# Kernel optimization log

Hardware: AMD Instinct MI355X
Metric: run time of the kernel (lower is better)

The kernel has to match this reference:

```python
import jax, jax.numpy as jnp
import numpy as np

NHEADS = 16

def setup_inputs() -> dict:
    key = jax.random.key(0)
    ks = jax.random.split(key, 11)
    B, S, D = 2, 2048, 1024
    std = 1.0 / np.sqrt(D)
    return {
        "query": jax.random.normal(ks[0], (B, S, D), jnp.float32),
        "key":   jax.random.normal(ks[1], (B, S, D), jnp.float32),
        "value": jax.random.normal(ks[2], (B, S, D), jnp.float32),
        "Wq": jax.random.normal(ks[3], (D, D), jnp.float32) * std,
        "bq": jax.random.normal(ks[4], (D,), jnp.float32) * std,
        "Wk": jax.random.normal(ks[5], (D, D), jnp.float32) * std,
        "bk": jax.random.normal(ks[6], (D,), jnp.float32) * std,
        "Wv": jax.random.normal(ks[7], (D, D), jnp.float32) * std,
        "bv": jax.random.normal(ks[8], (D,), jnp.float32) * std,
        "Wo": jax.random.normal(ks[9], (D, D), jnp.float32) * std,
        "bo": jax.random.normal(ks[10], (D,), jnp.float32) * std,
    }

def reference(query, key, value, Wq, bq, Wk, bk, Wv, bv, Wo, bo):
    B, Sq, D = query.shape
    Sk = key.shape[1]
    H = NHEADS
    hd = D // H
    q = (query @ Wq + bq).reshape(B, Sq, H, hd)
    k = (key @ Wk + bk).reshape(B, Sk, H, hd)
    v = (value @ Wv + bv).reshape(B, Sk, H, hd)
    # Explicit [B,H,Sq,Sk] score tensor, as in the original
    score = jnp.einsum('bqhd,bkhd->bhqk', q, k)
    # masked=True: causal mask applied before scaling (equivalent: -inf/c = -inf)
    cmask = jnp.triu(jnp.ones((Sq, Sk), dtype=bool), k=1)
    score = jnp.where(cmask, -jnp.inf, score)
    # NOTE: original divides by sqrt(score.shape[-1]) == sqrt(Sk), NOT sqrt(head_dim)
    scale = jnp.float32(1.0 / np.sqrt(Sk))
    att = jax.nn.softmax(score * scale, axis=-1)
    ret = jnp.einsum('bhqk,bkhd->bqhd', att, v).reshape(B, Sq, D)
    return ret @ Wo + bo
```

## Files before the change

kernel.cpp:

```cpp
#include <hip/hip_runtime.h>
#include <stdint.h>

typedef unsigned short u16;
typedef unsigned int u32;
typedef __bf16 bf16x8 __attribute__((ext_vector_type(8)));
typedef __bf16 bf16x4 __attribute__((ext_vector_type(4)));
typedef float f32x4 __attribute__((ext_vector_type(4)));

__device__ __forceinline__ u16 f2bf(float f) {
  u32 u = __float_as_uint(f);
  u = (u + 0x7fffu + ((u >> 16) & 1u)) >> 16;
  return (u16)u;
}

__device__ __forceinline__ void gload16(const void* g, void* l) {
  __builtin_amdgcn_global_load_lds(
      (const __attribute__((address_space(1))) void*)g,
      (__attribute__((address_space(3))) void*)l, 16, 0, 0);
}

__global__ __launch_bounds__(256) void prep_k(
    const float* __restrict__ q, const float* __restrict__ k,
    const float* __restrict__ v, u16* __restrict__ dst,
    const float* __restrict__ w0, const float* __restrict__ w1,
    const float* __restrict__ w2, const float* __restrict__ w3,
    u16* __restrict__ wt) {
  const int id = blockIdx.x;
  if (id < 6144) {
    const int y = id >> 11;
    const int x = id & 2047;
    const float* s = (y == 0) ? q : (y == 1) ? k : v;
    u16* d = dst + (size_t)y * 4194304u;
    int e = (x * 256 + threadIdx.x) * 8;
    float4 a = *(const float4*)(s + e);
    float4 b = *(const float4*)(s + e + 4);
    uint4 o;
    o.x = (u32)f2bf(a.x) | ((u32)f2bf(a.y) << 16);
    o.y = (u32)f2bf(a.z) | ((u32)f2bf(a.w) << 16);
    o.z = (u32)f2bf(b.x) | ((u32)f2bf(b.y) << 16);
    o.w = (u32)f2bf(b.z) | ((u32)f2bf(b.w) << 16);
    *(uint4*)(d + e) = o;
    return;
  }
  __shared__ float tile[64][65];
  const int t = id - 6144;
  const int z = t >> 8;
  const int rem = t & 255;
  const int x0 = (rem & 15) * 64, y0 = (rem >> 4) * 64;
  const float* W = (z == 0) ? w0 : (z == 1) ? w1 : (z == 2) ? w2 : w3;
  u16* Wt = wt + (size_t)z * 1048576u;
  const int tx = threadIdx.x & 63, ty = threadIdx.x >> 6;
#pragma unroll
  for (int j = 0; j < 16; ++j)
    tile[ty + j * 4][tx] = W[(size_t)(y0 + ty + j * 4) * 1024 + x0 + tx];
  __syncthreads();
#pragma unroll
  for (int j = 0; j < 16; ++j)
    Wt[(size_t)(x0 + ty + j * 4) * 1024 + y0 + tx] = f2bf(tile[tx][ty + j * 4]);
}

__global__ __launch_bounds__(256, 3) void gemm_proj(
    const u16* __restrict__ Xb, const u16* __restrict__ Wt,
    const float* __restrict__ bqp, const float* __restrict__ bkp,
    const float* __restrict__ bvp,
    u16* __restrict__ Qb, u16* __restrict__ Kb, u16* __restrict__ VtG,
    float qsc) {
  const int z = blockIdx.z;
  const u16 *A, *Bt;
  const float* bias;
  u16* C;
  int N, bm, bn;
  float osc = 1.f;
  bool rowb = false;
  if (z < 2) {
    A = Xb + (size_t)z * 4194304u;
    Bt = Wt + (size_t)z * 1048576u;
    bias = z ? bkp : bqp;
    C = z ? Kb : Qb;
    N = 1024;
    bm = blockIdx.x * 128;
    bn = blockIdx.y * 128;
    if (z == 0) osc = qsc;
  } else {
    A = Wt + 2u * 1048576u;
    Bt = Xb + 2u * 4194304u;
    bias = bvp;
    C = VtG;
    N = 4096;
    bm = blockIdx.y * 128;
    bn = blockIdx.x * 128;
    rowb = true;
  }

  __shared__ __align__(16) u16 ldsA[128 * 64];
  __shared__ __align__(16) u16 ldsB[128 * 64];

  const int tid = threadIdx.x;
  const int lane = tid & 63, wv = tid >> 6;
  const int wr = wv >> 1, wc = wv & 1;
  const int l15 = lane & 15, l4 = lane >> 4;

  const f32x4 zero4 = {0.f, 0.f, 0.f, 0.f};
  f32x4 acc[4][4];
#pragma unroll
  for (int i = 0; i < 4; ++i)
#pragma unroll
    for (int j = 0; j < 4; ++j) acc[i][j] = zero4;

  for (int kt = 0; kt < 16; ++kt) {
    __syncthreads();
#pragma unroll
    for (int g = 0; g < 4; ++g) {
      int p = g * 256 + tid;
      int row = p >> 3;
      int ss = (p & 7) ^ (row & 7);
      gload16(A + (size_t)(bm + row) * 1024 + kt * 64 + ss * 8,
              (char*)ldsA + (g * 256 + wv * 64) * 16);
    }
#pragma unroll
    for (int g = 0; g < 4; ++g) {
      int p = g * 256 + tid;
      int row = p >> 3;
      int ss = (p & 7) ^ (row & 7);
      gload16(Bt + (size_t)(bn + row) * 1024 + kt * 64 + ss * 8,
              (char*)ldsB + (g * 256 + wv * 64) * 16);
    }
    __syncthreads();

    bf16x8 af[4][2], bfr[4][2];
#pragma unroll
    for (int mf = 0; mf < 4; ++mf) {
      int row = wr * 64 + mf * 16 + l15;
#pragma unroll
      for (int ks = 0; ks < 2; ++ks) {
        int byt = row * 128 + ((ks * 64 + l4 * 16) ^ ((row & 7) << 4));
        af[mf][ks] = *(const bf16x8*)((const char*)ldsA + byt);
      }
    }
#pragma unroll
    for (int nf = 0; nf < 4; ++nf) {
      int row = wc * 64 + nf * 16 + l15;
#pragma unroll
      for (int ks = 0; ks < 2; ++ks) {
        int byt = row * 128 + ((ks * 64 + l4 * 16) ^ ((row & 7) << 4));
        bfr[nf][ks] = *(const bf16x8*)((const char*)ldsB + byt);
      }
    }
#pragma unroll
    for (int mf = 0; mf < 4; ++mf)
#pragma unroll
      for (int nf = 0; nf < 4; ++nf) {
        acc[mf][nf] = __builtin_amdgcn_mfma_f32_16x16x32_bf16(
            af[mf][0], bfr[nf][0], acc[mf][nf], 0, 0, 0);
        acc[mf][nf] = __builtin_amdgcn_mfma_f32_16x16x32_bf16(
            af[mf][1], bfr[nf][1], acc[mf][nf], 0, 0, 0);
      }
  }

  float bcol[4];
  if (!rowb) {
#pragma unroll
    for (int nf = 0; nf < 4; ++nf)
      bcol[nf] = bias[bn + wc * 64 + nf * 16 + l15];
  }
#pragma unroll
  for (int mf = 0; mf < 4; ++mf) {
#pragma unroll
    for (int i = 0; i < 4; ++i) {
      int r = bm + wr * 64 + mf * 16 + l4 * 4 + i;
      float br = rowb ? bias[r] : 0.f;
#pragma unroll
      for (int nf = 0; nf < 4; ++nf) {
        int c = bn + wc * 64 + nf * 16 + l15;
        float val = (acc[mf][nf][i] + (rowb ? br : bcol[nf])) * osc;
        C[(size_t)r * N + c] = f2bf(val);
      }
    }
  }
}

__global__ __launch_bounds__(256, 3) void gemm_out(
    const u16* __restrict__ A, const u16* __restrict__ Bt,
    const float* __restrict__ bias, float* __restrict__ C) {
  __shared__ __align__(16) u16 ldsA[128 * 64];
  __shared__ __align__(16) u16 ldsB[128 * 64];

  const int tid = threadIdx.x;
  const int lane = tid & 63, wv = tid >> 6;
  const int wr = wv >> 1, wc = wv & 1;
  const int l15 = lane & 15, l4 = lane >> 4;
  const int bm = blockIdx.x * 128, bn = blockIdx.y * 128;

  const f32x4 zero4 = {0.f, 0.f, 0.f, 0.f};
  f32x4 acc[4][4];
#pragma unroll
  for (int i = 0; i < 4; ++i)
#pragma unroll
    for (int j = 0; j < 4; ++j) acc[i][j] = zero4;

  for (int kt = 0; kt < 16; ++kt) {
    __syncthreads();
#pragma unroll
    for (int g = 0; g < 4; ++g) {
      int p = g * 256 + tid;
      int row = p >> 3;
      int ss = (p & 7) ^ (row & 7);
      gload16(A + (size_t)(bm + row) * 1024 + kt * 64 + ss * 8,
              (char*)ldsA + (g * 256 + wv * 64) * 16);
    }
#pragma unroll
    for (int g = 0; g < 4; ++g) {
      int p = g * 256 + tid;
      int row = p >> 3;
      int ss = (p & 7) ^ (row & 7);
      gload16(Bt + (size_t)(bn + row) * 1024 + kt * 64 + ss * 8,
              (char*)ldsB + (g * 256 + wv * 64) * 16);
    }
    __syncthreads();

    bf16x8 af[4][2], bfr[4][2];
#pragma unroll
    for (int mf = 0; mf < 4; ++mf) {
      int row = wr * 64 + mf * 16 + l15;
#pragma unroll
      for (int ks = 0; ks < 2; ++ks) {
        int byt = row * 128 + ((ks * 64 + l4 * 16) ^ ((row & 7) << 4));
        af[mf][ks] = *(const bf16x8*)((const char*)ldsA + byt);
      }
    }
#pragma unroll
    for (int nf = 0; nf < 4; ++nf) {
      int row = wc * 64 + nf * 16 + l15;
#pragma unroll
      for (int ks = 0; ks < 2; ++ks) {
        int byt = row * 128 + ((ks * 64 + l4 * 16) ^ ((row & 7) << 4));
        bfr[nf][ks] = *(const bf16x8*)((const char*)ldsB + byt);
      }
    }
#pragma unroll
    for (int mf = 0; mf < 4; ++mf)
#pragma unroll
      for (int nf = 0; nf < 4; ++nf) {
        acc[mf][nf] = __builtin_amdgcn_mfma_f32_16x16x32_bf16(
            af[mf][0], bfr[nf][0], acc[mf][nf], 0, 0, 0);
        acc[mf][nf] = __builtin_amdgcn_mfma_f32_16x16x32_bf16(
            af[mf][1], bfr[nf][1], acc[mf][nf], 0, 0, 0);
      }
  }

  float bcol[4];
#pragma unroll
  for (int nf = 0; nf < 4; ++nf)
    bcol[nf] = bias[bn + wc * 64 + nf * 16 + l15];
#pragma unroll
  for (int mf = 0; mf < 4; ++mf) {
#pragma unroll
    for (int i = 0; i < 4; ++i) {
      int r = bm + wr * 64 + mf * 16 + l4 * 4 + i;
#pragma unroll
      for (int nf = 0; nf < 4; ++nf) {
        int c = bn + wc * 64 + nf * 16 + l15;
        C[(size_t)r * 1024 + c] = acc[mf][nf][i] + bcol[nf];
      }
    }
  }
}

__global__ __launch_bounds__(256, 4) void attn_k(
    const u16* __restrict__ Q, const u16* __restrict__ Kb,
    const u16* __restrict__ Vt, u16* __restrict__ ctx) {
  const int id = blockIdx.x + (blockIdx.y << 5);
  const int xcd = id & 7;
  const int kk = id >> 3;
  const int bh = xcd * 4 + (kk & 3);
  const int qt = 31 - (kk >> 2);
  const int b = bh >> 4, h = bh & 15;
  const int tid = threadIdx.x;
  const int lane = tid & 63, wv = tid >> 6;
  const int l15 = lane & 15, l4 = lane >> 4;

  __shared__ __align__(16) u16 Kt[2][64 * 64];
  __shared__ __align__(16) u16 Vl[2][64 * 64];
  __shared__ __align__(16) u16 Pl[4][16 * 64];

  const u16* KB = Kb + (size_t)(b * 2048) * 1024 + h * 64;
  const u16* VB = Vt + (size_t)(h * 64) * 4096 + b * 2048;

  const u16* qp =
      Q + (size_t)(b * 2048 + qt * 64 + wv * 16 + l15) * 1024 + h * 64;
  bf16x8 qf0 = *(const bf16x8*)(qp + l4 * 8);
  bf16x8 qf1 = *(const bf16x8*)(qp + 32 + l4 * 8);

  const f32x4 zero4 = {0.f, 0.f, 0.f, 0.f};
  f32x4 oacc[4];
#pragma unroll
  for (int i = 0; i < 4; ++i) oacc[i] = zero4;
  float m = -1e30f, lsum = 0.f;

  auto issueKV = [&](int jt, int bufi) {
    const u16* kb = KB + (size_t)(jt * 64) * 1024;
#pragma unroll
    for (int g = 0; g < 2; ++g) {
      int p = g * 256 + tid;
      int row = p >> 3;
      int ss = (p & 7) ^ (row & 7);
      gload16(kb + (size_t)row * 1024 + ss * 8,
              (char*)(&Kt[bufi][0]) + (g * 256 + wv * 64) * 16);
    }
#pragma unroll
    for (int g = 0; g < 2; ++g) {
      int p = g * 256 + tid;
      int d = p >> 3;
      int ss = (p & 7) ^ (d & 7);
      gload16(VB + (size_t)d * 4096 + jt * 64 + ss * 8,
              (char*)(&Vl[bufi][0]) + (g * 256 + wv * 64) * 16);
    }
  };

  issueKV(0, 0);
  for (int j = 0; j <= qt; ++j) {
    const int cur = j & 1;
    __syncthreads();
    if (j < qt) issueKV(j + 1, cur ^ 1);

    f32x4 p4[4];
    __builtin_amdgcn_s_setprio(1);
#pragma unroll
    for (int nt = 0; nt < 4; ++nt) {
      int row = nt * 16 + l15;
      int sw = (row & 7) << 4;
      const char* kr = (const char*)&Kt[cur][0] + row * 128;
      bf16x8 k0 = *(const bf16x8*)(kr + ((l4 * 16) ^ sw));
      bf16x8 k1 = *(const bf16x8*)(kr + ((64 + l4 * 16) ^ sw));
      f32x4 s = zero4;
      s = __builtin_amdgcn_mfma_f32_16x16x32_bf16(k0, qf0, s, 0, 0, 0);
      s = __builtin_amdgcn_mfma_f32_16x16x32_bf16(k1, qf1, s, 0, 0, 0);
      p4[nt] = s;
    }
    __builtin_amdgcn_s_setprio(0);

    if (j == qt) {
#pragma unroll
      for (int nt = 0; nt < 4; ++nt)
#pragma unroll
        for (int i = 0; i < 4; ++i)
          if (nt * 16 + l4 * 4 + i > wv * 16 + l15) p4[nt][i] = -1e30f;
    }

    float rm = p4[0][0];
#pragma unroll
    for (int nt = 0; nt < 4; ++nt)
#pragma unroll
      for (int i = 0; i < 4; ++i) rm = fmaxf(rm, p4[nt][i]);
    rm = fmaxf(rm, __shfl_xor(rm, 16, 64));
    rm = fmaxf(rm, __shfl_xor(rm, 32, 64));

    if (!__all(rm - m <= 8.0f)) {
      float mn = fmaxf(m, rm);
      float ce = exp2f(m - mn);
      m = mn;
      lsum *= ce;
#pragma unroll
      for (int i = 0; i < 4; ++i) {
        float cei = __shfl(ce, (lane & 48) | (l4 * 4 + i), 64);
#pragma unroll
        for (int nt = 0; nt < 4; ++nt) oacc[nt][i] *= cei;
      }
    }

    float rs = 0.f;
#pragma unroll
    for (int nt = 0; nt < 4; ++nt)
#pragma unroll
      for (int i = 0; i < 4; ++i) {
        float e = exp2f(p4[nt][i] - m);
        p4[nt][i] = e;
        rs += e;
      }
    rs += __shfl_xor(rs, 16, 64);
    rs += __shfl_xor(rs, 32, 64);
    lsum += rs;

    {
      int sw = (l15 & 7) << 4;
#pragma unroll
      for (int nt = 0; nt < 4; ++nt) {
        bf16x4 pb = __builtin_convertvector(p4[nt], bf16x4);
        *(bf16x4*)((char*)&Pl[wv][0] + l15 * 128 + ((nt * 32 + l4 * 8) ^ sw)) = pb;
      }
    }

    bf16x8 pa0, pa1;
    {
      int sw = (l15 & 7) << 4;
      pa0 = *(const bf16x8*)((const char*)&Pl[wv][0] + l15 * 128 + ((l4 * 16) ^ sw));
      pa1 = *(const bf16x8*)((const char*)&Pl[wv][0] + l15 * 128 +
                             ((64 + l4 * 16) ^ sw));
    }
    __builtin_amdgcn_s_setprio(1);
#pragma unroll
    for (int nt = 0; nt < 4; ++nt) {
      int d = nt * 16 + l15;
      int sw = (d & 7) << 4;
      const char* vr = (const char*)&Vl[cur][0] + d * 128;
      bf16x8 v0 = *(const bf16x8*)(vr + ((l4 * 16) ^ sw));
      bf16x8 v1 = *(const bf16x8*)(vr + ((64 + l4 * 16) ^ sw));
      oacc[nt] = __builtin_amdgcn_mfma_f32_16x16x32_bf16(pa0, v0, oacc[nt], 0, 0, 0);
      oacc[nt] = __builtin_amdgcn_mfma_f32_16x16x32_bf16(pa1, v1, oacc[nt], 0, 0, 0);
    }
    __builtin_amdgcn_s_setprio(0);
  }

  float rcp = 1.f / lsum;
  u16* cb = ctx + (size_t)(b * 2048 + qt * 64 + wv * 16) * 1024 + h * 64;
#pragma unroll
  for (int i = 0; i < 4; ++i) {
    float iv = __shfl(rcp, (lane & 48) | (l4 * 4 + i), 64);
    int r = l4 * 4 + i;
#pragma unroll
    for (int nt = 0; nt < 4; ++nt)
      cb[(size_t)r * 1024 + nt * 16 + l15] = f2bf(oacc[nt][i] * iv);
  }
}

extern "C" void kernel_launch(void* const* d_in, const int* in_sizes, int n_in,
                              void* d_out, int out_size, void* d_ws,
                              size_t ws_size, hipStream_t stream) {
  const float* q  = (const float*)d_in[0];
  const float* k  = (const float*)d_in[1];
  const float* v  = (const float*)d_in[2];
  const float* Wq = (const float*)d_in[3];
  const float* bq = (const float*)d_in[4];
  const float* Wk = (const float*)d_in[5];
  const float* bk = (const float*)d_in[6];
  const float* Wv = (const float*)d_in[7];
  const float* bv = (const float*)d_in[8];
  const float* Wo = (const float*)d_in[9];
  const float* bo = (const float*)d_in[10];

  char* ws = (char*)d_ws;
  u16* Xb  = (u16*)ws;
  u16* Wt  = (u16*)(ws + 25165824);
  u16* VtG = (u16*)(ws + 33554432);
  u16* ctx = Xb;
  u16* Qb  = (u16*)d_out;
  u16* Kb  = Qb + 4194304;

  const float SC2A = 0.0318793585f;

  prep_k<<<dim3(7168), 256, 0, stream>>>(q, k, v, Xb, Wq, Wk, Wv, Wo, Wt);
  gemm_proj<<<dim3(32, 8, 3), 256, 0, stream>>>(Xb, Wt, bq, bk, bv, Qb, Kb,
                                                VtG, SC2A);
  attn_k<<<dim3(32, 32), 256, 0, stream>>>(Qb, Kb, VtG, ctx);
  gemm_out<<<dim3(32, 8), 256, 0, stream>>>(ctx, Wt + 3 * 1048576, bo,
                                            (float*)d_out);
}
```

Before: 114.2 us.

## Load K and V fragments directly from global memory instead of LDS staging

Removes the double-buffered LDS staging of K and V tiles (async global-to-LDS copies plus a barrier per iteration) and has each wave read its MFMA operand fragments straight from global memory. This drops the per-iteration __syncthreads and the LDS footprint, which could raise occupancy. In exchange, the four waves of a block each fetch the same K/V data separately, relying on cache, and the loads are no longer prefetched ahead of the compute, which exposes global-memory latency.

```diff
diff --git a/kernel.cpp b/kernel.cpp
--- a/kernel.cpp
+++ b/kernel.cpp
@@ -279,8 +279,6 @@
   const int lane = tid & 63, wv = tid >> 6;
   const int l15 = lane & 15, l4 = lane >> 4;
 
-  __shared__ __align__(16) u16 Kt[2][64 * 64];
-  __shared__ __align__(16) u16 Vl[2][64 * 64];
   __shared__ __align__(16) u16 Pl[4][16 * 64];
 
   const u16* KB = Kb + (size_t)(b * 2048) * 1024 + h * 64;
@@ -297,41 +295,14 @@
   for (int i = 0; i < 4; ++i) oacc[i] = zero4;
   float m = -1e30f, lsum = 0.f;
 
-  auto issueKV = [&](int jt, int bufi) {
-    const u16* kb = KB + (size_t)(jt * 64) * 1024;
-#pragma unroll
-    for (int g = 0; g < 2; ++g) {
-      int p = g * 256 + tid;
-      int row = p >> 3;
-      int ss = (p & 7) ^ (row & 7);
-      gload16(kb + (size_t)row * 1024 + ss * 8,
-              (char*)(&Kt[bufi][0]) + (g * 256 + wv * 64) * 16);
-    }
-#pragma unroll
-    for (int g = 0; g < 2; ++g) {
-      int p = g * 256 + tid;
-      int d = p >> 3;
-      int ss = (p & 7) ^ (d & 7);
-      gload16(VB + (size_t)d * 4096 + jt * 64 + ss * 8,
-              (char*)(&Vl[bufi][0]) + (g * 256 + wv * 64) * 16);
-    }
-  };
-
-  issueKV(0, 0);
   for (int j = 0; j <= qt; ++j) {
-    const int cur = j & 1;
-    __syncthreads();
-    if (j < qt) issueKV(j + 1, cur ^ 1);
-
     f32x4 p4[4];
     __builtin_amdgcn_s_setprio(1);
 #pragma unroll
     for (int nt = 0; nt < 4; ++nt) {
-      int row = nt * 16 + l15;
-      int sw = (row & 7) << 4;
-      const char* kr = (const char*)&Kt[cur][0] + row * 128;
-      bf16x8 k0 = *(const bf16x8*)(kr + ((l4 * 16) ^ sw));
-      bf16x8 k1 = *(const bf16x8*)(kr + ((64 + l4 * 16) ^ sw));
+      const u16* kr = KB + (size_t)(j * 64 + nt * 16 + l15) * 1024;
+      bf16x8 k0 = *(const bf16x8*)(kr + l4 * 8);
+      bf16x8 k1 = *(const bf16x8*)(kr + 32 + l4 * 8);
       f32x4 s = zero4;
       s = __builtin_amdgcn_mfma_f32_16x16x32_bf16(k0, qf0, s, 0, 0, 0);
       s = __builtin_amdgcn_mfma_f32_16x16x32_bf16(k1, qf1, s, 0, 0, 0);
@@ -400,11 +371,9 @@
     __builtin_amdgcn_s_setprio(1);
 #pragma unroll
     for (int nt = 0; nt < 4; ++nt) {
-      int d = nt * 16 + l15;
-      int sw = (d & 7) << 4;
-      const char* vr = (const char*)&Vl[cur][0] + d * 128;
-      bf16x8 v0 = *(const bf16x8*)(vr + ((l4 * 16) ^ sw));
-      bf16x8 v1 = *(const bf16x8*)(vr + ((64 + l4 * 16) ^ sw));
+      const u16* vr = VB + (size_t)(nt * 16 + l15) * 4096 + j * 64;
+      bf16x8 v0 = *(const bf16x8*)(vr + l4 * 8);
+      bf16x8 v1 = *(const bf16x8*)(vr + 32 + l4 * 8);
       oacc[nt] = __builtin_amdgcn_mfma_f32_16x16x32_bf16(pa0, v0, oacc[nt], 0, 0, 0);
       oacc[nt] = __builtin_amdgcn_mfma_f32_16x16x32_bf16(pa1, v1, oacc[nt], 0, 0, 0);
     }
```

Measured after the change: 210.7 us. 84.5% more time.

## Pair causal query tiles per block to balance work and share K/V loads

Applied to the files above, without the earlier changes.

Each attention block now handles two query tiles, qtA and its mirror 31-qtA, so every block does the same total causal work. The K/V tiles it loads are reused by both tiles for the shared prefix. The grid is halved to 512 blocks and launch bounds drop to 2 blocks per CU to make room for the doubled accumulators. This removes the tail imbalance of causal tiles and cuts redundant K/V traffic, at the cost of fewer resident waves and higher register pressure.

```diff
diff --git a/kernel.cpp b/kernel.cpp
--- a/kernel.cpp
+++ b/kernel.cpp
@@ -266,14 +266,15 @@
   }
 }
 
-__global__ __launch_bounds__(256, 4) void attn_k(
+__global__ __launch_bounds__(256, 2) void attn_k(
     const u16* __restrict__ Q, const u16* __restrict__ Kb,
     const u16* __restrict__ Vt, u16* __restrict__ ctx) {
-  const int id = blockIdx.x + (blockIdx.y << 5);
+  const int id = blockIdx.x + (blockIdx.y << 4);
   const int xcd = id & 7;
   const int kk = id >> 3;
   const int bh = xcd * 4 + (kk & 3);
-  const int qt = 31 - (kk >> 2);
+  const int qtA = kk >> 2;
+  const int qtB = 31 - qtA;
   const int b = bh >> 4, h = bh & 15;
   const int tid = threadIdx.x;
   const int lane = tid & 63, wv = tid >> 6;
@@ -286,16 +287,20 @@
   const u16* KB = Kb + (size_t)(b * 2048) * 1024 + h * 64;
   const u16* VB = Vt + (size_t)(h * 64) * 4096 + b * 2048;
 
-  const u16* qp =
-      Q + (size_t)(b * 2048 + qt * 64 + wv * 16 + l15) * 1024 + h * 64;
-  bf16x8 qf0 = *(const bf16x8*)(qp + l4 * 8);
-  bf16x8 qf1 = *(const bf16x8*)(qp + 32 + l4 * 8);
+  const u16* qpa =
+      Q + (size_t)(b * 2048 + qtA * 64 + wv * 16 + l15) * 1024 + h * 64;
+  const u16* qpb =
+      Q + (size_t)(b * 2048 + qtB * 64 + wv * 16 + l15) * 1024 + h * 64;
+  bf16x8 qa0 = *(const bf16x8*)(qpa + l4 * 8);
+  bf16x8 qa1 = *(const bf16x8*)(qpa + 32 + l4 * 8);
+  bf16x8 qb0 = *(const bf16x8*)(qpb + l4 * 8);
+  bf16x8 qb1 = *(const bf16x8*)(qpb + 32 + l4 * 8);
 
   const f32x4 zero4 = {0.f, 0.f, 0.f, 0.f};
-  f32x4 oacc[4];
-#pragma unroll
-  for (int i = 0; i < 4; ++i) oacc[i] = zero4;
-  float m = -1e30f, lsum = 0.f;
+  f32x4 oA[4], oB[4];
+#pragma unroll
+  for (int i = 0; i < 4; ++i) { oA[i] = zero4; oB[i] = zero4; }
+  float mA = -1e30f, lsA = 0.f, mB = -1e30f, lsB = 0.f;
 
   auto issueKV = [&](int jt, int bufi) {
     const u16* kb = KB + (size_t)(jt * 64) * 1024;
@@ -317,12 +322,8 @@
     }
   };
 
-  issueKV(0, 0);
-  for (int j = 0; j <= qt; ++j) {
-    const int cur = j & 1;
-    __syncthreads();
-    if (j < qt) issueKV(j + 1, cur ^ 1);
-
+  auto computeTile = [&](int cur, bool diag, bf16x8 qf0, bf16x8 qf1,
+                         float& m, float& lsum, f32x4* oacc) {
     f32x4 p4[4];
     __builtin_amdgcn_s_setprio(1);
 #pragma unroll
@@ -339,7 +340,7 @@
     }
     __builtin_amdgcn_s_setprio(0);
 
-    if (j == qt) {
+    if (diag) {
 #pragma unroll
       for (int nt = 0; nt < 4; ++nt)
 #pragma unroll
@@ -409,17 +410,32 @@
       oacc[nt] = __builtin_amdgcn_mfma_f32_16x16x32_bf16(pa1, v1, oacc[nt], 0, 0, 0);
     }
     __builtin_amdgcn_s_setprio(0);
-  }
-
-  float rcp = 1.f / lsum;
-  u16* cb = ctx + (size_t)(b * 2048 + qt * 64 + wv * 16) * 1024 + h * 64;
+  };
+
+  issueKV(0, 0);
+  for (int j = 0; j <= qtB; ++j) {
+    const int cur = j & 1;
+    __syncthreads();
+    if (j < qtB) issueKV(j + 1, cur ^ 1);
+    computeTile(cur, j == qtB, qb0, qb1, mB, lsB, oB);
+    if (j <= qtA) computeTile(cur, j == qtA, qa0, qa1, mA, lsA, oA);
+  }
+
+  float rcpA = 1.f / lsA;
+  float rcpB = 1.f / lsB;
+  u16* ca = ctx + (size_t)(b * 2048 + qtA * 64 + wv * 16) * 1024 + h * 64;
+  u16* cb = ctx + (size_t)(b * 2048 + qtB * 64 + wv * 16) * 1024 + h * 64;
 #pragma unroll
   for (int i = 0; i < 4; ++i) {
-    float iv = __shfl(rcp, (lane & 48) | (l4 * 4 + i), 64);
+    int src = (lane & 48) | (l4 * 4 + i);
+    float ivA = __shfl(rcpA, src, 64);
+    float ivB = __shfl(rcpB, src, 64);
     int r = l4 * 4 + i;
 #pragma unroll
-    for (int nt = 0; nt < 4; ++nt)
-      cb[(size_t)r * 1024 + nt * 16 + l15] = f2bf(oacc[nt][i] * iv);
+    for (int nt = 0; nt < 4; ++nt) {
+      ca[(size_t)r * 1024 + nt * 16 + l15] = f2bf(oA[nt][i] * ivA);
+      cb[(size_t)r * 1024 + nt * 16 + l15] = f2bf(oB[nt][i] * ivB);
+    }
   }
 }
 
@@ -451,7 +467,7 @@
   prep_k<<<dim3(7168), 256, 0, stream>>>(q, k, v, Xb, Wq, Wk, Wv, Wo, Wt);
   gemm_proj<<<dim3(32, 8, 3), 256, 0, stream>>>(Xb, Wt, bq, bk, bv, Qb, Kb,
                                                 VtG, SC2A);
-  attn_k<<<dim3(32, 32), 256, 0, stream>>>(Qb, Kb, VtG, ctx);
+  attn_k<<<dim3(16, 32), 256, 0, stream>>>(Qb, Kb, VtG, ctx);
   gemm_out<<<dim3(32, 8), 256, 0, stream>>>(ctx, Wt + 3 * 1048576, bo,
                                             (float*)d_out);
 }
```

After: 114.4 us. About the same (+0.2%).

## Split KV range for long causal query tiles and merge with combine kernel

Applied to the files above, without the earlier changes.

Each of the longer query tiles (qt 16..31) is now processed by two attention blocks, each covering half of its key/value tiles. The split blocks write unnormalized fp32 partial outputs plus row max and sum to workspace, and a new combine kernel merges them with softmax rescaling into bf16 context. The goal is to cut the causal load imbalance, where the last tiles loop up to 32 times while early tiles loop once, so the critical path shrinks. In exchange it adds an extra kernel launch and roughly 16MB of fp32 partial-output traffic. The scratch space reuses workspace regions, including the Wq slot of the transposed weights, which is already consumed by the time attention runs.

```diff
diff --git a/kernel.cpp b/kernel.cpp
--- a/kernel.cpp
+++ b/kernel.cpp
@@ -268,12 +268,28 @@
 
 __global__ __launch_bounds__(256, 4) void attn_k(
     const u16* __restrict__ Q, const u16* __restrict__ Kb,
-    const u16* __restrict__ Vt, u16* __restrict__ ctx) {
-  const int id = blockIdx.x + (blockIdx.y << 5);
+    const u16* __restrict__ Vt, u16* __restrict__ ctx,
+    float* __restrict__ Opart, float* __restrict__ ML) {
+  const int id = blockIdx.x;
   const int xcd = id & 7;
   const int kk = id >> 3;
   const int bh = xcd * 4 + (kk & 3);
-  const int qt = 31 - (kk >> 2);
+  const int t = kk >> 2;
+  int qt, j0, j1, seg = 0;
+  bool split;
+  if (t < 32) {
+    split = true;
+    qt = 31 - (t >> 1);
+    seg = t & 1;
+    int half = (qt + 1) >> 1;
+    j0 = seg ? half : 0;
+    j1 = seg ? (qt + 1) : half;
+  } else {
+    split = false;
+    qt = 47 - t;
+    j0 = 0;
+    j1 = qt + 1;
+  }
   const int b = bh >> 4, h = bh & 15;
   const int tid = threadIdx.x;
   const int lane = tid & 63, wv = tid >> 6;
@@ -317,11 +333,11 @@
     }
   };
 
-  issueKV(0, 0);
-  for (int j = 0; j <= qt; ++j) {
-    const int cur = j & 1;
+  issueKV(j0, 0);
+  for (int j = j0; j < j1; ++j) {
+    const int cur = (j - j0) & 1;
     __syncthreads();
-    if (j < qt) issueKV(j + 1, cur ^ 1);
+    if (j + 1 < j1) issueKV(j + 1, cur ^ 1);
 
     f32x4 p4[4];
     __builtin_amdgcn_s_setprio(1);
@@ -411,15 +427,70 @@
     __builtin_amdgcn_s_setprio(0);
   }
 
-  float rcp = 1.f / lsum;
-  u16* cb = ctx + (size_t)(b * 2048 + qt * 64 + wv * 16) * 1024 + h * 64;
-#pragma unroll
-  for (int i = 0; i < 4; ++i) {
-    float iv = __shfl(rcp, (lane & 48) | (l4 * 4 + i), 64);
-    int r = l4 * 4 + i;
-#pragma unroll
-    for (int nt = 0; nt < 4; ++nt)
-      cb[(size_t)r * 1024 + nt * 16 + l15] = f2bf(oacc[nt][i] * iv);
+  if (!split) {
+    float rcp = 1.f / lsum;
+    u16* cb = ctx + (size_t)(b * 2048 + qt * 64 + wv * 16) * 1024 + h * 64;
+#pragma unroll
+    for (int i = 0; i < 4; ++i) {
+      float iv = __shfl(rcp, (lane & 48) | (l4 * 4 + i), 64);
+      int r = l4 * 4 + i;
+#pragma unroll
+      for (int nt = 0; nt < 4; ++nt)
+        cb[(size_t)r * 1024 + nt * 16 + l15] = f2bf(oacc[nt][i] * iv);
+    }
+  } else {
+    const int gidx = (bh * 16 + (qt - 16)) * 2 + seg;
+    float* Ob = Opart + (size_t)gidx * 4096;
+#pragma unroll
+    for (int i = 0; i < 4; ++i) {
+      int r = wv * 16 + l4 * 4 + i;
+#pragma unroll
+      for (int nt = 0; nt < 4; ++nt) Ob[r * 64 + nt * 16 + l15] = oacc[nt][i];
+    }
+    if (l4 == 0) {
+      float* mlb = ML + (size_t)gidx * 128;
+      mlb[(wv * 16 + l15) * 2] = m;
+      mlb[(wv * 16 + l15) * 2 + 1] = lsum;
+    }
+  }
+}
+
+__global__ __launch_bounds__(256) void combine_k(
+    const float* __restrict__ Opart, const float* __restrict__ ML,
+    u16* __restrict__ ctx) {
+  const int id = blockIdx.x;
+  const int xcd = id & 7;
+  const int rest = id >> 3;
+  const int bh = xcd * 4 + (rest & 3);
+  const int qq = rest >> 2;
+  const int qt = 16 + qq;
+  const int b = bh >> 4, h = bh & 15;
+  const int g = bh * 16 + qq;
+  const float* O0 = Opart + (size_t)(g * 2) * 4096;
+  const float* O1 = O0 + 4096;
+  const float* ml0 = ML + (size_t)(g * 2) * 128;
+  const float* ml1 = ml0 + 128;
+
+  const int r = threadIdx.x >> 2;
+  const int c0 = (threadIdx.x & 3) * 16;
+  float m0 = ml0[r * 2], l0 = ml0[r * 2 + 1];
+  float m1 = ml1[r * 2], l1 = ml1[r * 2 + 1];
+  float mm = fmaxf(m0, m1);
+  float w0 = exp2f(m0 - mm), w1 = exp2f(m1 - mm);
+  float inv = 1.f / (l0 * w0 + l1 * w1);
+  w0 *= inv;
+  w1 *= inv;
+  u16* cb = ctx + (size_t)(b * 2048 + qt * 64 + r) * 1024 + h * 64 + c0;
+#pragma unroll
+  for (int c = 0; c < 16; c += 4) {
+    float4 a = *(const float4*)(O0 + r * 64 + c0 + c);
+    float4 bb = *(const float4*)(O1 + r * 64 + c0 + c);
+    u32 lo = (u32)f2bf(a.x * w0 + bb.x * w1) |
+             ((u32)f2bf(a.y * w0 + bb.y * w1) << 16);
+    u32 hi = (u32)f2bf(a.z * w0 + bb.z * w1) |
+             ((u32)f2bf(a.w * w0 + bb.w * w1) << 16);
+    uint2 pk = {lo, hi};
+    *(uint2*)(cb + c) = pk;
   }
 }
 
@@ -439,10 +510,12 @@
   const float* bo = (const float*)d_in[10];
 
   char* ws = (char*)d_ws;
-  u16* Xb  = (u16*)ws;
-  u16* Wt  = (u16*)(ws + 25165824);
-  u16* VtG = (u16*)(ws + 33554432);
-  u16* ctx = Xb;
+  u16* Xb    = (u16*)ws;
+  u16* Wt    = (u16*)(ws + 25165824);
+  u16* VtG   = (u16*)(ws + 33554432);
+  u16* ctx   = Xb;
+  float* Opart = (float*)(ws + 8388608);
+  float* ML    = (float*)(ws + 25165824);
   u16* Qb  = (u16*)d_out;
   u16* Kb  = Qb + 4194304;
 
@@ -451,7 +524,8 @@
   prep_k<<<dim3(7168), 256, 0, stream>>>(q, k, v, Xb, Wq, Wk, Wv, Wo, Wt);
   gemm_proj<<<dim3(32, 8, 3), 256, 0, stream>>>(Xb, Wt, bq, bk, bv, Qb, Kb,
                                                 VtG, SC2A);
-  attn_k<<<dim3(32, 32), 256, 0, stream>>>(Qb, Kb, VtG, ctx);
+  attn_k<<<dim3(1536), 256, 0, stream>>>(Qb, Kb, VtG, ctx, Opart, ML);
+  combine_k<<<dim3(512), 256, 0, stream>>>(Opart, ML, ctx);
   gemm_out<<<dim3(32, 8), 256, 0, stream>>>(ctx, Wt + 3 * 1048576, bo,
                                             (float*)d_out);
 }
```

Measured after the change: 123.7 us. 1.08x slower.
